# Kernel tuning notes

Hardware: AMD Instinct MI355X
Metric: run time of the kernel (lower is better)

## Reference

```python
import jax, jax.numpy as jnp
import numpy as np

N_ITEMS = 100000
DIM = 64
N_EDGES = 3200000  # ~32 avg degree
BATCH = 4096


def setup_inputs() -> dict:
    key = jax.random.key(0)
    k1, k2, k3, k4, k5, k6, k7 = jax.random.split(key, 7)
    item_feature = jax.random.normal(k1, (N_ITEMS, DIM), dtype=jnp.float32) * 0.1
    # normalized-laplacian-like edge weights (small positive values ~ 1/deg)
    edge_vals = jax.random.uniform(k2, (N_EDGES,), dtype=jnp.float32) * (1.0 / 32.0)
    edge_rows = jax.random.randint(k3, (N_EDGES,), 0, N_ITEMS, dtype=jnp.int32)
    edge_cols = jax.random.randint(k4, (N_EDGES,), 0, N_ITEMS, dtype=jnp.int32)
    idx = jax.random.randint(k5, (BATCH,), 0, N_ITEMS, dtype=jnp.int32)
    i_pos = jax.random.randint(k6, (BATCH,), 0, N_ITEMS, dtype=jnp.int32)
    i_neg = jax.random.randint(k7, (BATCH,), 0, N_ITEMS, dtype=jnp.int32)
    return {"item_feature": item_feature, "edge_vals": edge_vals,
            "edge_rows": edge_rows, "edge_cols": edge_cols,
            "idx": idx, "i_pos": i_pos, "i_neg": i_neg}


def reference(item_feature, edge_vals, edge_rows, edge_cols, idx, i_pos, i_neg):
    # propagate(): (sparse_graph @ item_feature + item_feature) / 2
    # SpMM as gather-scale-scatter over COO edges.
    msg = item_feature[edge_cols] * edge_vals[:, None]              # [E, D]
    agg = jax.ops.segment_sum(msg, edge_rows,
                              num_segments=item_feature.shape[0])   # [N, D]
    prop = (agg + item_feature) * 0.5                                # [N, D]

    item_feat = prop[idx]    # [B, D]
    pos_feat = prop[i_pos]   # [B, D]
    neg_feat = prop[i_neg]   # [B, D]

    # full pairwise scores [B, B], as in the original (item_feat @ pos_feat.T)
    diff = jnp.einsum('bd,cd->bc', item_feat, pos_feat) \
         - jnp.einsum('bd,cd->bc', item_feat, neg_feat)
    # -log(sigmoid(x)) computed stably
    loss = -jnp.mean(jax.nn.log_sigmoid(diff))
    return loss
```

## Files before the change

kernel.cpp:

```cpp
#include <hip/hip_runtime.h>
#include <hip/hip_bf16.h>

#define DIM 64
#define NBUK 8
#define CAPX 32
#define SBITS_WORDS 3200

typedef __attribute__((ext_vector_type(8))) short short8;
typedef __attribute__((ext_vector_type(4))) float f32x4;

__device__ __forceinline__ unsigned short f2bf(float f) {
  unsigned int u = __float_as_uint(f);
  u = (u + 0x7FFFu + ((u >> 16) & 1u)) >> 16;
  return (unsigned short)u;
}
__device__ __forceinline__ float bf2f(unsigned short h) {
  return __uint_as_float(((unsigned)h) << 16);
}

#define SF_STRIDE 8
#define RD_STRIDE 16

#define VSCALE 1048576.0f
#define VINV (1.0f / 1048576.0f)

__global__ void prep_kernel(const int* __restrict__ idx,
                            const int* __restrict__ ipos,
                            const int* __restrict__ ineg, int Bn,
                            int* __restrict__ counts,
                            unsigned long long* __restrict__ sum_fixed,
                            int* __restrict__ row_done, int* __restrict__ gdone,
                            int nrows, const float4* __restrict__ feat4,
                            short8* __restrict__ featb8, int nFeat8) {
  int t = blockIdx.x * blockDim.x + threadIdx.x;
  if (t < 3 * Bn) {
    int r = (t < Bn) ? idx[t] : (t < 2 * Bn ? ipos[t - Bn] : ineg[t - 2 * Bn]);
    int4* c4 = (int4*)(counts + (size_t)r * NBUK);
    c4[0] = make_int4(0, 0, 0, 0);
    c4[1] = make_int4(0, 0, 0, 0);
    int u = t;
    if (u < nrows * SF_STRIDE) sum_fixed[u] = 0ULL;
    if (u < nrows * RD_STRIDE) row_done[u] = 0;
    if (u == 0) *gdone = 0;
  }
  if (t < nFeat8) {
    float4 a = feat4[2 * t];
    float4 b = feat4[2 * t + 1];
    short8 v;
    v[0] = (short)f2bf(a.x); v[1] = (short)f2bf(a.y);
    v[2] = (short)f2bf(a.z); v[3] = (short)f2bf(a.w);
    v[4] = (short)f2bf(b.x); v[5] = (short)f2bf(b.y);
    v[6] = (short)f2bf(b.z); v[7] = (short)f2bf(b.w);
    featb8[t] = v;
  }
}

__global__ __launch_bounds__(1024) void scatter3_kernel(
    const int4* __restrict__ er4, const int4* __restrict__ ec4,
    const float4* __restrict__ ev4, const int4* __restrict__ idx4,
    const int4* __restrict__ ipos4, const int4* __restrict__ ineg4, int Bn4,
    int* __restrict__ counts, unsigned* __restrict__ lists, int E8, int E) {
  __shared__ unsigned sbits[SBITS_WORDS];
  for (int i = threadIdx.x; i < SBITS_WORDS; i += 1024) sbits[i] = 0u;
  __syncthreads();
  for (int i = threadIdx.x; i < Bn4; i += 1024) {
    int4 a = idx4[i];
    int4 b = ipos4[i];
    int4 c = ineg4[i];
    atomicOr(&sbits[((unsigned)a.x) >> 5], 1u << (a.x & 31));
    atomicOr(&sbits[((unsigned)a.y) >> 5], 1u << (a.y & 31));
    atomicOr(&sbits[((unsigned)a.z) >> 5], 1u << (a.z & 31));
    atomicOr(&sbits[((unsigned)a.w) >> 5], 1u << (a.w & 31));
    atomicOr(&sbits[((unsigned)b.x) >> 5], 1u << (b.x & 31));
    atomicOr(&sbits[((unsigned)b.y) >> 5], 1u << (b.y & 31));
    atomicOr(&sbits[((unsigned)b.z) >> 5], 1u << (b.z & 31));
    atomicOr(&sbits[((unsigned)b.w) >> 5], 1u << (b.w & 31));
    atomicOr(&sbits[((unsigned)c.x) >> 5], 1u << (c.x & 31));
    atomicOr(&sbits[((unsigned)c.y) >> 5], 1u << (c.y & 31));
    atomicOr(&sbits[((unsigned)c.z) >> 5], 1u << (c.z & 31));
    atomicOr(&sbits[((unsigned)c.w) >> 5], 1u << (c.w & 31));
  }
  __syncthreads();

  int buk = blockIdx.x & (NBUK - 1);
  int i = blockIdx.x * blockDim.x + threadIdx.x;
  if (i < E8) {
    int4 r0 = er4[2 * i];
    int4 r1 = er4[2 * i + 1];
    int rr[8] = {r0.x, r0.y, r0.z, r0.w, r1.x, r1.y, r1.z, r1.w};
    unsigned m[8];
    unsigned any = 0;
#pragma unroll
    for (int k = 0; k < 8; ++k) {
      m[k] = (sbits[((unsigned)rr[k]) >> 5] >> (rr[k] & 31)) & 1u;
      any |= m[k];
    }
    if (any) {
      int4 c0 = ec4[2 * i];
      int4 c1 = ec4[2 * i + 1];
      float4 v0 = ev4[2 * i];
      float4 v1 = ev4[2 * i + 1];
      int cc[8] = {c0.x, c0.y, c0.z, c0.w, c1.x, c1.y, c1.z, c1.w};
      float vv[8] = {v0.x, v0.y, v0.z, v0.w, v1.x, v1.y, v1.z, v1.w};
#pragma unroll
      for (int k = 0; k < 8; ++k) {
        if (m[k]) {
          int r = rr[k];
          int p = atomicAdd(&counts[(size_t)r * NBUK + buk], 1);
          if (p < CAPX) {
            unsigned pv = __float2uint_rn(vv[k] * VSCALE);
            lists[((size_t)r * NBUK + buk) * CAPX + p] =
                (pv << 17) | (unsigned)cc[k];
          }
        }
      }
    }
  }
  if (i == 0) {
    const int* er = (const int*)er4;
    const int* ec = (const int*)ec4;
    const float* ev = (const float*)ev4;
    for (int e = (E >> 3) << 3; e < E; ++e) {
      int r = er[e];
      if ((sbits[((unsigned)r) >> 5] >> (r & 31)) & 1u) {
        int p = atomicAdd(&counts[(size_t)r * NBUK + buk], 1);
        if (p < CAPX) {
          unsigned pv = __float2uint_rn(ev[e] * VSCALE);
          lists[((size_t)r * NBUK + buk) * CAPX + p] =
              (pv << 17) | (unsigned)ec[e];
        }
      }
    }
  }
}

__global__ __launch_bounds__(256, 2) void accum_build_kernel(
    const int* __restrict__ counts, const unsigned* __restrict__ lists,
    const unsigned short* __restrict__ featb, const int* __restrict__ idx,
    const int* __restrict__ ipos, const int* __restrict__ ineg,
    unsigned short* __restrict__ A, unsigned short* __restrict__ Bm, int Bn) {
  int wv = (blockIdx.x * blockDim.x + threadIdx.x) >> 6;
  int lane = threadIdx.x & 63;

  auto gather = [&](int r) -> float {
    const int4* c4 = (const int4*)(counts + (size_t)r * NBUK);
    int4 ca = c4[0];
    int4 cb = c4[1];
    int n[NBUK] = {ca.x, ca.y, ca.z, ca.w, cb.x, cb.y, cb.z, cb.w};
    int jmax = 0;
#pragma unroll
    for (int x = 0; x < NBUK; ++x) {
      n[x] = n[x] > CAPX ? CAPX : n[x];
      jmax = n[x] > jmax ? n[x] : jmax;
    }
    const unsigned* base = lists + (size_t)r * NBUK * CAPX;
    float acc0 = 0.0f, acc1 = 0.0f;
    unsigned ecur[NBUK];
#pragma unroll
    for (int x = 0; x < NBUK; ++x) ecur[x] = base[x * CAPX];
    for (int j = 0; j < jmax; ++j) {
      unsigned enext[NBUK];
#pragma unroll
      for (int x = 0; x < NBUK; ++x)
        enext[x] = base[x * CAPX + j + 1];
#pragma unroll
      for (int x = 0; x < NBUK; ++x) {
        bool valid = j < n[x];
        int col = valid ? (int)(ecur[x] & 0x1FFFFu) : 0;
        float val = valid ? (float)(ecur[x] >> 17) * VINV : 0.0f;
        float f = bf2f(featb[(size_t)col * DIM + lane]);
        if (x & 1)
          acc1 = fmaf(val, f, acc1);
        else
          acc0 = fmaf(val, f, acc0);
      }
#pragma unroll
      for (int x = 0; x < NBUK; ++x) ecur[x] = enext[x];
    }
    return 0.5f * (acc0 + acc1 + bf2f(featb[(size_t)r * DIM + lane]));
  };

  if (wv < Bn) {
    int b = wv;
    float v = gather(idx[b]);
    A[((size_t)((b >> 4) * 8 + (lane >> 3))) * 128 + (b & 15) * 8 + (lane & 7)] =
        f2bf(v);
  } else if (wv < 2 * Bn) {
    int j = wv - Bn;
    float v = gather(ipos[j]) - gather(ineg[j]);
    Bm[((size_t)((j >> 4) * 8 + (lane >> 3))) * 128 + (j & 15) * 8 + (lane & 7)] =
        f2bf(v);
  }
}

__global__ __launch_bounds__(256) void gemm_loss_kernel(
    const short8* __restrict__ A, const short8* __restrict__ Bm,
    unsigned long long* __restrict__ sum_fixed, int* __restrict__ row_done,
    int* __restrict__ gdone, float* __restrict__ out, double inv) {
  int t = threadIdx.x;
  int lane = t & 63;
  int w = t >> 6;
  int wr = w >> 1;
  int wc = w & 1;
  int frow = lane & 15;
  int hi = lane >> 4;

  int ablk = blockIdx.y * 8 + wr * 4;
  int bblk = blockIdx.x * 8 + wc * 4;

  f32x4 acc[4][4];
#pragma unroll
  for (int m = 0; m < 4; ++m)
#pragma unroll
    for (int n = 0; n < 4; ++n) acc[m][n] = (f32x4){0.f, 0.f, 0.f, 0.f};

#pragma unroll
  for (int kk = 0; kk < 2; ++kk) {
    short8 a[4], b[4];
#pragma unroll
    for (int m = 0; m < 4; ++m)
      a[m] = A[((ablk + m) * 8 + kk * 4 + hi) * 16 + frow];
#pragma unroll
    for (int n = 0; n < 4; ++n)
      b[n] = Bm[((bblk + n) * 8 + kk * 4 + hi) * 16 + frow];
#pragma unroll
    for (int m = 0; m < 4; ++m)
#pragma unroll
      for (int n = 0; n < 4; ++n)
        acc[m][n] = __builtin_amdgcn_mfma_f32_16x16x32_bf16(a[m], b[n],
                                                            acc[m][n], 0, 0, 0);
  }

  float local = 0.0f;
#pragma unroll
  for (int m = 0; m < 4; ++m)
#pragma unroll
    for (int n = 0; n < 4; ++n)
#pragma unroll
      for (int i = 0; i < 4; ++i) {
        float z = -acc[m][n][i];
        float az = fabsf(z);
        local += fmaxf(z, 0.0f) + __logf(1.0f + __expf(-az));
      }
#pragma unroll
  for (int off = 32; off > 0; off >>= 1) local += __shfl_down(local, off, 64);

  __shared__ float red[4];
  if (lane == 0) red[w] = local;
  __syncthreads();

  if (w == 0) {
    int last = 0;
    if (lane == 0) {
      double bs = (double)red[0] + red[1] + red[2] + red[3];
      long long f = (long long)llrint(bs * 1048576.0);
      unsigned long long old =
          atomicAdd(&sum_fixed[blockIdx.y * SF_STRIDE], (unsigned long long)f);
      int inc = 1 | (int)(old >> 63);
      int pos = atomicAdd(&row_done[blockIdx.y * RD_STRIDE], inc);
      if (pos == (int)gridDim.x - 1) {
        int g = atomicAdd(gdone, 1);
        last = (g == (int)gridDim.y - 1);
      }
    }
    last = __shfl(last, 0, 64);
    if (last) {
      long long part = 0;
      if (lane < (int)gridDim.y)
        part = (long long)atomicAdd(&sum_fixed[lane * SF_STRIDE], 0ULL);
#pragma unroll
      for (int off = 32; off > 0; off >>= 1)
        part += __shfl_down(part, off, 64);
      if (lane == 0)
        out[0] = (float)((double)part * inv * (1.0 / 1048576.0));
    }
  }
}

extern "C" void kernel_launch(void* const* d_in, const int* in_sizes, int n_in,
                              void* d_out, int out_size, void* d_ws,
                              size_t ws_size, hipStream_t stream) {
  const float* feat = (const float*)d_in[0];
  const float* evals = (const float*)d_in[1];
  const int* erows = (const int*)d_in[2];
  const int* ecols = (const int*)d_in[3];
  const int* idx = (const int*)d_in[4];
  const int* ipos = (const int*)d_in[5];
  const int* ineg = (const int*)d_in[6];
  float* out = (float*)d_out;

  int nItems = in_sizes[0] / DIM;
  int E = in_sizes[1];
  int Bn = in_sizes[4];

  char* w = (char*)d_ws;
  size_t off = 0;
  auto alloc = [&](size_t bytes) -> void* {
    void* p = w + off;
    off += (bytes + 255) & ~(size_t)255;
    return p;
  };
  int* counts = (int*)alloc((size_t)nItems * NBUK * 4);
  unsigned* lists =
      (unsigned*)alloc((size_t)nItems * NBUK * CAPX * 4 + 2048);
  unsigned short* featb = (unsigned short*)alloc((size_t)nItems * DIM * 2);
  unsigned short* Amat = (unsigned short*)alloc((size_t)Bn * DIM * 2);
  unsigned short* Bmat = (unsigned short*)alloc((size_t)Bn * DIM * 2);
  int gx = Bn / 128;
  unsigned long long* sum_fixed =
      (unsigned long long*)alloc((size_t)gx * SF_STRIDE * 8);
  int* row_done = (int*)alloc((size_t)gx * RD_STRIDE * 4);
  int* gdone = (int*)alloc(64);

  int nFeat8 = nItems * DIM / 8;
  int prepThreads = nFeat8 > 3 * Bn ? nFeat8 : 3 * Bn;
  prep_kernel<<<(prepThreads + 255) / 256, 256, 0, stream>>>(
      idx, ipos, ineg, Bn, counts, sum_fixed, row_done, gdone, gx,
      (const float4*)feat, (short8*)featb, nFeat8);

  int E8 = E / 8;
  scatter3_kernel<<<512, 1024, 0, stream>>>(
      (const int4*)erows, (const int4*)ecols, (const float4*)evals,
      (const int4*)idx, (const int4*)ipos, (const int4*)ineg, Bn / 4, counts,
      lists, E8, E);

  int nWaves = 2 * Bn;
  accum_build_kernel<<<(nWaves * 64 + 255) / 256, 256, 0, stream>>>(
      counts, lists, featb, idx, ipos, ineg, Amat, Bmat, Bn);

  double inv = 1.0 / ((double)Bn * (double)Bn);
  gemm_loss_kernel<<<dim3(gx, gx), 256, 0, stream>>>(
      (const short8*)Amat, (const short8*)Bmat, sum_fixed, row_done, gdone,
      out, inv);
}
```

Before: 73.48 us.

## Software-pipeline feature gathers, split pos/neg gathers into separate waves

The gather loop now prefetches feature values one step ahead, alongside the edge entries, so global-load latency overlaps the FMAs. The pos and neg gathers move to separate waves (3*Bn waves instead of 2*Bn), which balances work per wave and adds parallelism. Launch bounds rise to 4 blocks per CU. The subtraction pos-neg moves into the GEMM kernel, which now reads two B matrices and converts bf16 to fp32 and back per element. That adds GEMM load traffic and ALU work, and changes rounding because each term is rounded to bf16 before subtracting.

```diff
diff --git a/kernel.cpp b/kernel.cpp
--- a/kernel.cpp
+++ b/kernel.cpp
@@ -134,11 +134,12 @@
   }
 }
 
-__global__ __launch_bounds__(256, 2) void accum_build_kernel(
+__global__ __launch_bounds__(256, 4) void accum_build_kernel(
     const int* __restrict__ counts, const unsigned* __restrict__ lists,
     const unsigned short* __restrict__ featb, const int* __restrict__ idx,
     const int* __restrict__ ipos, const int* __restrict__ ineg,
-    unsigned short* __restrict__ A, unsigned short* __restrict__ Bm, int Bn) {
+    unsigned short* __restrict__ A, unsigned short* __restrict__ P,
+    unsigned short* __restrict__ Nm, int Bn) {
   int wv = (blockIdx.x * blockDim.x + threadIdx.x) >> 6;
   int lane = threadIdx.x & 63;
 
@@ -155,46 +156,66 @@
     }
     const unsigned* base = lists + (size_t)r * NBUK * CAPX;
     float acc0 = 0.0f, acc1 = 0.0f;
-    unsigned ecur[NBUK];
-#pragma unroll
-    for (int x = 0; x < NBUK; ++x) ecur[x] = base[x * CAPX];
+    unsigned e0[NBUK], e1[NBUK];
+    float f0[NBUK];
+#pragma unroll
+    for (int x = 0; x < NBUK; ++x) {
+      e0[x] = base[x * CAPX];
+      e1[x] = base[x * CAPX + 1];
+    }
+#pragma unroll
+    for (int x = 0; x < NBUK; ++x) {
+      int col = (0 < n[x]) ? (int)(e0[x] & 0x1FFFFu) : 0;
+      f0[x] = bf2f(featb[(size_t)col * DIM + lane]);
+    }
     for (int j = 0; j < jmax; ++j) {
-      unsigned enext[NBUK];
+      unsigned e2[NBUK];
+      float f1[NBUK];
 #pragma unroll
       for (int x = 0; x < NBUK; ++x)
-        enext[x] = base[x * CAPX + j + 1];
+        e2[x] = base[x * CAPX + j + 2];
 #pragma unroll
       for (int x = 0; x < NBUK; ++x) {
-        bool valid = j < n[x];
-        int col = valid ? (int)(ecur[x] & 0x1FFFFu) : 0;
-        float val = valid ? (float)(ecur[x] >> 17) * VINV : 0.0f;
-        float f = bf2f(featb[(size_t)col * DIM + lane]);
+        int col = (j + 1 < n[x]) ? (int)(e1[x] & 0x1FFFFu) : 0;
+        f1[x] = bf2f(featb[(size_t)col * DIM + lane]);
+      }
+#pragma unroll
+      for (int x = 0; x < NBUK; ++x) {
+        float val = (j < n[x]) ? (float)(e0[x] >> 17) * VINV : 0.0f;
         if (x & 1)
-          acc1 = fmaf(val, f, acc1);
+          acc1 = fmaf(val, f0[x], acc1);
         else
-          acc0 = fmaf(val, f, acc0);
-      }
-#pragma unroll
-      for (int x = 0; x < NBUK; ++x) ecur[x] = enext[x];
+          acc0 = fmaf(val, f0[x], acc0);
+      }
+#pragma unroll
+      for (int x = 0; x < NBUK; ++x) {
+        e0[x] = e1[x];
+        e1[x] = e2[x];
+        f0[x] = f1[x];
+      }
     }
     return 0.5f * (acc0 + acc1 + bf2f(featb[(size_t)r * DIM + lane]));
   };
 
-  if (wv < Bn) {
-    int b = wv;
-    float v = gather(idx[b]);
-    A[((size_t)((b >> 4) * 8 + (lane >> 3))) * 128 + (b & 15) * 8 + (lane & 7)] =
-        f2bf(v);
-  } else if (wv < 2 * Bn) {
-    int j = wv - Bn;
-    float v = gather(ipos[j]) - gather(ineg[j]);
-    Bm[((size_t)((j >> 4) * 8 + (lane >> 3))) * 128 + (j & 15) * 8 + (lane & 7)] =
-        f2bf(v);
+  if (wv < 3 * Bn) {
+    int b, r;
+    unsigned short* dst;
+    if (wv < Bn) {
+      b = wv; r = idx[b]; dst = A;
+    } else if (wv < 2 * Bn) {
+      b = wv - Bn; r = ipos[b]; dst = P;
+    } else {
+      b = wv - 2 * Bn; r = ineg[b]; dst = Nm;
+    }
+    float v = gather(r);
+    dst[((size_t)((b >> 4) * 8 + (lane >> 3))) * 128 + (b & 15) * 8 +
+        (lane & 7)] = f2bf(v);
   }
 }
 
 __global__ __launch_bounds__(256) void gemm_loss_kernel(
-    const short8* __restrict__ A, const short8* __restrict__ Bm,
+    const short8* __restrict__ A, const short8* __restrict__ P,
+    const short8* __restrict__ Nm,
     unsigned long long* __restrict__ sum_fixed, int* __restrict__ row_done,
     int* __restrict__ gdone, float* __restrict__ out, double inv) {
   int t = threadIdx.x;
@@ -221,8 +242,16 @@
     for (int m = 0; m < 4; ++m)
       a[m] = A[((ablk + m) * 8 + kk * 4 + hi) * 16 + frow];
 #pragma unroll
-    for (int n = 0; n < 4; ++n)
-      b[n] = Bm[((bblk + n) * 8 + kk * 4 + hi) * 16 + frow];
+    for (int n = 0; n < 4; ++n) {
+      short8 p = P[((bblk + n) * 8 + kk * 4 + hi) * 16 + frow];
+      short8 q = Nm[((bblk + n) * 8 + kk * 4 + hi) * 16 + frow];
+      short8 d;
+#pragma unroll
+      for (int i = 0; i < 8; ++i)
+        d[i] = (short)f2bf(bf2f((unsigned short)p[i]) -
+                           bf2f((unsigned short)q[i]));
+      b[n] = d;
+    }
 #pragma unroll
     for (int m = 0; m < 4; ++m)
 #pragma unroll
@@ -305,7 +334,8 @@
       (unsigned*)alloc((size_t)nItems * NBUK * CAPX * 4 + 2048);
   unsigned short* featb = (unsigned short*)alloc((size_t)nItems * DIM * 2);
   unsigned short* Amat = (unsigned short*)alloc((size_t)Bn * DIM * 2);
-  unsigned short* Bmat = (unsigned short*)alloc((size_t)Bn * DIM * 2);
+  unsigned short* Pmat = (unsigned short*)alloc((size_t)Bn * DIM * 2);
+  unsigned short* Nmat = (unsigned short*)alloc((size_t)Bn * DIM * 2);
   int gx = Bn / 128;
   unsigned long long* sum_fixed =
       (unsigned long long*)alloc((size_t)gx * SF_STRIDE * 8);
@@ -324,12 +354,12 @@
       (const int4*)idx, (const int4*)ipos, (const int4*)ineg, Bn / 4, counts,
       lists, E8, E);
 
-  int nWaves = 2 * Bn;
+  int nWaves = 3 * Bn;
   accum_build_kernel<<<(nWaves * 64 + 255) / 256, 256, 0, stream>>>(
-      counts, lists, featb, idx, ipos, ineg, Amat, Bmat, Bn);
+      counts, lists, featb, idx, ipos, ineg, Amat, Pmat, Nmat, Bn);
 
   double inv = 1.0 / ((double)Bn * (double)Bn);
   gemm_loss_kernel<<<dim3(gx, gx), 256, 0, stream>>>(
-      (const short8*)Amat, (const short8*)Bmat, sum_fixed, row_done, gdone,
-      out, inv);
-}
+      (const short8*)Amat, (const short8*)Pmat, (const short8*)Nmat, sum_fixed,
+      row_done, gdone, out, inv);
+}
```

Result: slower. 77.13 us (+5.0%).
